# Performance work log

Hardware: AMD Instinct MI355X
Metric: run time of the kernel (lower is better)

Reference implementation:

```python
import jax, jax.numpy as jnp
import numpy as np

DEPTH = 3  # chemprop default message passing depth


def setup_inputs() -> dict:
    key = jax.random.key(0)
    ks = jax.random.split(key, 10)
    n_atoms, n_bonds, max_nb, n_mols = 50000, 100000, 6, 2000
    atom_fdim, bond_fdim, hidden = 133, 147, 300
    f_atoms = jax.random.normal(ks[0], (n_atoms, atom_fdim), dtype=jnp.float32)
    f_bonds = jax.random.normal(ks[1], (n_bonds, bond_fdim), dtype=jnp.float32)
    a2b = jax.random.randint(ks[2], (n_atoms, max_nb), 0, n_bonds, dtype=jnp.int32)
    b2a = jax.random.randint(ks[3], (n_bonds,), 0, n_atoms, dtype=jnp.int32)
    b2revb = jax.random.randint(ks[4], (n_bonds,), 0, n_bonds, dtype=jnp.int32)
    mol_id = jnp.sort(jax.random.randint(ks[5], (n_atoms,), 0, n_mols, dtype=jnp.int32))
    W_i = jax.random.normal(ks[6], (bond_fdim, hidden), dtype=jnp.float32) * 0.05
    W_h = jax.random.normal(ks[7], (hidden, hidden), dtype=jnp.float32) * 0.05
    W_o = jax.random.normal(ks[8], (atom_fdim + hidden, hidden), dtype=jnp.float32) * 0.05
    b_o = jnp.zeros((hidden,), dtype=jnp.float32)
    return {"f_atoms": f_atoms, "f_bonds": f_bonds, "a2b": a2b, "b2a": b2a,
            "b2revb": b2revb, "mol_id": mol_id, "n_mols": n_mols,
            "W_i": W_i, "W_h": W_h, "W_o": W_o, "b_o": b_o}


def reference(f_atoms, f_bonds, a2b, b2a, b2revb, mol_id, n_mols, W_i, W_h, W_o, b_o):
    act = jax.nn.relu
    # W_i: bond features -> hidden; message init
    inp = f_bonds @ W_i                      # [n_bonds, h]
    message = act(inp)
    for _ in range(DEPTH - 1):
        nei = message[a2b]                    # [n_atoms, max_nb, h] gather
        a_message = nei.sum(axis=1)           # [n_atoms, h]
        rev = message[b2revb]                 # [n_bonds, h]
        message = a_message[b2a] - rev        # [n_bonds, h]
        message = act(inp + message @ W_h)
    # final atom readout
    a_message = message[a2b].sum(axis=1)      # [n_atoms, h]
    a_input = jnp.concatenate([f_atoms, a_message], axis=1)  # [n_atoms, fa+h]
    atom_hiddens = act(a_input @ W_o + b_o)   # [n_atoms, h]
    # ragged per-molecule mean (a_scope loop -> segment mean)
    sums = jax.ops.segment_sum(atom_hiddens, mol_id, num_segments=n_mols)
    counts = jax.ops.segment_sum(jnp.ones((atom_hiddens.shape[0],), dtype=atom_hiddens.dtype), mol_id, num_segments=n_mols)
    mol_vecs = jnp.where(counts[:, None] > 0, sums / jnp.maximum(counts, 1.0)[:, None], 0.0)
    return mol_vecs
```

## Files before the change

### kernel.cpp

```cpp
#include <hip/hip_runtime.h>
#include <cstddef>

#define H 300
#define RS 304
#define MAXNB 6
#define ASTR 312

typedef __attribute__((ext_vector_type(8)))  short bf16x8;
typedef __attribute__((ext_vector_type(16))) float f32x16;

__device__ __forceinline__ float bf2f(unsigned short u) {
    return __uint_as_float(((unsigned int)u) << 16);
}
__device__ __forceinline__ unsigned short f2bf(float f) {
    unsigned int u = __float_as_uint(f);
    u += 0x7FFFu + ((u >> 16) & 1u);
    return (unsigned short)(u >> 16);
}
__device__ __forceinline__ unsigned int sub2bf(unsigned int a, unsigned int b) {
    float d0 = bf2f((unsigned short)(a & 0xFFFFu)) - bf2f((unsigned short)(b & 0xFFFFu));
    float d1 = bf2f((unsigned short)(a >> 16))     - bf2f((unsigned short)(b >> 16));
    return (unsigned int)f2bf(d0) | ((unsigned int)f2bf(d1) << 16);
}
__device__ __forceinline__ unsigned int relu2(unsigned int w) {
    unsigned int r = w;
    if (w & 0x80000000u) r &= 0x0000FFFFu;
    if (w & 0x00008000u) r &= 0xFFFF0000u;
    return r;
}
__device__ __forceinline__ uint4 relu4(uint4 v) {
    v.x = relu2(v.x); v.y = relu2(v.y); v.z = relu2(v.z); v.w = relu2(v.w);
    return v;
}
__device__ __forceinline__ uint4 subpack4(uint4 a, uint4 b) {
    uint4 r;
    r.x = sub2bf(a.x, b.x); r.y = sub2bf(a.y, b.y);
    r.z = sub2bf(a.z, b.z); r.w = sub2bf(a.w, b.w);
    return r;
}


template<int S>
__global__ void __launch_bounds__(256)
pack_a_f32_c(const float* __restrict__ src, unsigned short* __restrict__ dst,
             int M, int K)
{
    __shared__ unsigned short sm[64 * 152];
    const int m0 = blockIdx.x * 64;
    const int r = threadIdx.x >> 2;
    const int q = threadIdx.x & 3;
    int mv = m0 + r; if (mv >= M) mv = M - 1;
    const float* rowF = src + (size_t)mv * K;
#pragma unroll
    for (int i = 0; i < (S * 4 + 3) / 4; ++i) {
        int c = q + i * 4;
        if (c * 4 < S * 16) {
            unsigned short h[4];
#pragma unroll
            for (int e = 0; e < 4; ++e) {
                int k = c * 4 + e;
                h[e] = (k < K) ? f2bf(rowF[k]) : (unsigned short)0;
            }
            uint2 o;
            o.x = (unsigned int)h[0] | ((unsigned int)h[1] << 16);
            o.y = (unsigned int)h[2] | ((unsigned int)h[3] << 16);
            *(uint2*)&sm[r * 152 + c * 4] = o;
        }
    }
    __syncthreads();
    for (int j = threadIdx.x; j < 2 * S * 64; j += 256) {
        int lane = j & 63;
        int t = j >> 6;
        int s = t % S;
        int mb2 = t / S;
        uint4 v = *(const uint4*)&sm[(mb2 * 32 + (lane & 31)) * 152 + s * 16 + (lane >> 5) * 8];
        int m_blk = blockIdx.x * 2 + mb2;
        *(uint4*)&dst[((size_t)(m_blk * S + s) * 64 + lane) * 8] = v;
    }
}

__global__ void __launch_bounds__(256)
pack_b(const float* __restrict__ src1, const float* __restrict__ src2,
       unsigned short* __restrict__ dst, int K1, int S1, int K2, int SB)
{
    int g = blockIdx.x * 256 + threadIdx.x;
    if (g >= 10 * SB * 64) return;
    int lane = g & 63;
    int t = g >> 6;
    int s = t % SB;
    int n_blk = t / SB;
    int n = n_blk * 32 + (lane & 31);
    unsigned int w[4];
#pragma unroll
    for (int p = 0; p < 4; ++p) {
        unsigned short h[2];
#pragma unroll
        for (int e = 0; e < 2; ++e) {
            int kf = s * 16 + (lane >> 5) * 8 + p * 2 + e;
            float v = 0.0f;
            if (n < H) {
                if (s < S1) {
                    if (kf < K1) v = src1[(size_t)kf * H + n];
                } else {
                    int k2 = kf - S1 * 16;
                    if (k2 < K2) v = src2[(size_t)k2 * H + n];
                }
            }
            h[e] = f2bf(v);
        }
        w[p] = (unsigned int)h[0] | ((unsigned int)h[1] << 16);
    }
    *(uint4*)&dst[(size_t)g * 8] = make_uint4(w[0], w[1], w[2], w[3]);
}

template<int RELU>
__global__ void __launch_bounds__(256)
aggregate_row(const unsigned short* __restrict__ msg, const int* __restrict__ a2b,
              unsigned short* __restrict__ amsg, int n_atoms)
{
    int gid = blockIdx.x * 256 + threadIdx.x;
    int total = n_atoms * 38;
    if (gid >= total) return;
    int atom = gid / 38;
    int g8 = gid - atom * 38;
    const int* nb = a2b + atom * MAXNB;
    float sum[8] = {};
#pragma unroll
    for (int j = 0; j < MAXNB; ++j) {
        int b = nb[j];
        uint4 v = *(const uint4*)&msg[(size_t)b * RS + g8 * 8];
        if (RELU) v = relu4(v);
        unsigned int ww[4] = {v.x, v.y, v.z, v.w};
#pragma unroll
        for (int p = 0; p < 4; ++p) {
            sum[p * 2]     += bf2f((unsigned short)(ww[p] & 0xFFFFu));
            sum[p * 2 + 1] += bf2f((unsigned short)(ww[p] >> 16));
        }
    }
    unsigned int ow[4];
#pragma unroll
    for (int p = 0; p < 4; ++p)
        ow[p] = (unsigned int)f2bf(sum[p * 2]) | ((unsigned int)f2bf(sum[p * 2 + 1]) << 16);
    *(uint4*)&amsg[(size_t)atom * RS + g8 * 8] = make_uint4(ow[0], ow[1], ow[2], ow[3]);
}

template<int S1, int S2, int SBL, int MODE, int RELUMSG>
__global__ void __launch_bounds__(128)
gemm_fused(const unsigned short* __restrict__ A1,
           const unsigned short* __restrict__ amsg,
           const unsigned short* __restrict__ msg,
           const int* __restrict__ b2a, const int* __restrict__ b2revb,
           const unsigned short* __restrict__ Bp,
           const float* __restrict__ bias,
           const unsigned short* __restrict__ inp_add,
           const float* __restrict__ Adense, int Kd,
           unsigned short* __restrict__ out, int M)
{
    __shared__ __align__(16) unsigned short smem[32 * ASTR];

    const int lane  = threadIdx.x & 63;
    const int w     = threadIdx.x >> 6;
    const int cbase = w * 160;
    const int mrow  = lane & 31;
    const int quad  = lane >> 5;
    const int m0    = blockIdx.x * 32;
    const int m_blk = blockIdx.x;
    const int nblk0 = cbase >> 5;

    {
        const int r = threadIdx.x >> 2;
        const int q = threadIdx.x & 3;
        int mm = m0 + r;
        int mv = (mm < M) ? mm : 0;
        if (MODE == 0) {
            if (mm >= M) mv = M - 1;
            const float* rowF = Adense + (size_t)mv * Kd;
#pragma unroll
            for (int i = 0; i < (S2 * 4 + 3) / 4; ++i) {
                int c = q + i * 4;
                if (c * 4 < S2 * 16) {
                    unsigned short h[4];
#pragma unroll
                    for (int e = 0; e < 4; ++e) {
                        int k = c * 4 + e;
                        h[e] = (k < Kd) ? f2bf(rowF[k]) : (unsigned short)0;
                    }
                    uint2 o;
                    o.x = (unsigned int)h[0] | ((unsigned int)h[1] << 16);
                    o.y = (unsigned int)h[2] | ((unsigned int)h[3] << 16);
                    *(uint2*)&smem[r * ASTR + c * 4] = o;
                }
            }
            __syncthreads();
        } else if (MODE == 1 || MODE == 2) {
            const unsigned short* rowA;
            const unsigned short* rowM = nullptr;
            if (MODE == 1) {
                rowA = amsg + (size_t)b2a[mv] * RS;
                rowM = msg  + (size_t)b2revb[mv] * RS;
            } else {
                rowA = amsg + (size_t)mv * RS;
            }
#pragma unroll
            for (int i = 0; i < 10; ++i) {
                int c = q + i * 4;
                if (c < 38) {
                    uint4 o;
                    if (MODE == 1) {
                        uint4 va = *(const uint4*)(rowA + c * 8);
                        uint4 vm = *(const uint4*)(rowM + c * 8);
                        if (RELUMSG) vm = relu4(vm);
                        o = subpack4(va, vm);
                    } else {
                        o = *(const uint4*)(rowA + c * 8);
                    }
                    *(uint4*)&smem[r * ASTR + c * 8] = o;
                }
            }
            __syncthreads();
        }
    }

    f32x16 acc[5];
#pragma unroll
    for (int t = 0; t < 5; ++t)
#pragma unroll
        for (int i = 0; i < 16; ++i) acc[t][i] = 0.0f;

    const unsigned short* pa1 = (S1 > 0) ? (A1 + ((size_t)m_blk * S1 * 64 + lane) * 8) : nullptr;
    const unsigned short* pb  = Bp + ((size_t)nblk0 * SBL * 64 + lane) * 8;

    constexpr int STOT = S1 + S2;

    auto loadA = [&](int s) -> bf16x8 {
        if (s < S1) return *(const bf16x8*)(pa1 + (size_t)s * 512);
        return *(const bf16x8*)&smem[mrow * ASTR + (s - S1) * 16 + quad * 8];
    };

    bf16x8 b0[5], b1[5];
#pragma unroll
    for (int nt = 0; nt < 5; ++nt) b0[nt] = *(const bf16x8*)(pb + ((size_t)nt * SBL + 0) * 512);
    if (STOT > 1) {
#pragma unroll
        for (int nt = 0; nt < 5; ++nt) b1[nt] = *(const bf16x8*)(pb + ((size_t)nt * SBL + 1) * 512);
    }

#pragma unroll
    for (int s = 0; s < STOT; s += 2) {
        bf16x8 a = loadA(s);
        acc[0] = __builtin_amdgcn_mfma_f32_32x32x16_bf16(a, b0[0], acc[0], 0, 0, 0);
        acc[1] = __builtin_amdgcn_mfma_f32_32x32x16_bf16(a, b0[1], acc[1], 0, 0, 0);
        acc[2] = __builtin_amdgcn_mfma_f32_32x32x16_bf16(a, b0[2], acc[2], 0, 0, 0);
        acc[3] = __builtin_amdgcn_mfma_f32_32x32x16_bf16(a, b0[3], acc[3], 0, 0, 0);
        acc[4] = __builtin_amdgcn_mfma_f32_32x32x16_bf16(a, b0[4], acc[4], 0, 0, 0);
        if (s + 2 < STOT) {
#pragma unroll
            for (int nt = 0; nt < 5; ++nt) b0[nt] = *(const bf16x8*)(pb + ((size_t)nt * SBL + s + 2) * 512);
        }
        if (s + 1 < STOT) {
            bf16x8 a2 = loadA(s + 1);
            acc[0] = __builtin_amdgcn_mfma_f32_32x32x16_bf16(a2, b1[0], acc[0], 0, 0, 0);
            acc[1] = __builtin_amdgcn_mfma_f32_32x32x16_bf16(a2, b1[1], acc[1], 0, 0, 0);
            acc[2] = __builtin_amdgcn_mfma_f32_32x32x16_bf16(a2, b1[2], acc[2], 0, 0, 0);
            acc[3] = __builtin_amdgcn_mfma_f32_32x32x16_bf16(a2, b1[3], acc[3], 0, 0, 0);
            acc[4] = __builtin_amdgcn_mfma_f32_32x32x16_bf16(a2, b1[4], acc[4], 0, 0, 0);
            if (s + 3 < STOT) {
#pragma unroll
                for (int nt = 0; nt < 5; ++nt) b1[nt] = *(const bf16x8*)(pb + ((size_t)nt * SBL + s + 3) * 512);
            }
        }
    }

    __syncthreads();

#pragma unroll
    for (int nt = 0; nt < 5; ++nt) {
        int col = cbase + nt * 32 + mrow;
#pragma unroll
        for (int r = 0; r < 16; ++r) {
            int row = (r & 3) + 8 * (r >> 2) + 4 * quad;
            if (col < 308) smem[row * 308 + col] = f2bf(acc[nt][r]);
        }
    }
    __syncthreads();

    for (int idx = threadIdx.x; idx < 32 * 76; idx += 128) {
        int row = idx / 76, gcol = idx - row * 76;
        int mm = m0 + row;
        if (mm >= M) continue;
        int c0 = gcol * 4;
        uint2 raw = *(const uint2*)&smem[row * 308 + c0];
        uint2 o;
        if (MODE == 0) {
            o = raw;
        } else {
            unsigned short h[4] = {(unsigned short)(raw.x & 0xFFFFu), (unsigned short)(raw.x >> 16),
                                   (unsigned short)(raw.y & 0xFFFFu), (unsigned short)(raw.y >> 16)};
            float v[4];
#pragma unroll
            for (int e = 0; e < 4; ++e) v[e] = bf2f(h[e]);
            if (MODE == 1) {
                uint2 iv = *(const uint2*)&inp_add[(size_t)mm * RS + c0];
                v[0] += bf2f((unsigned short)(iv.x & 0xFFFFu));
                v[1] += bf2f((unsigned short)(iv.x >> 16));
                v[2] += bf2f((unsigned short)(iv.y & 0xFFFFu));
                v[3] += bf2f((unsigned short)(iv.y >> 16));
            } else {
#pragma unroll
                for (int e = 0; e < 4; ++e) v[e] += (c0 + e < H) ? bias[c0 + e] : 0.0f;
            }
#pragma unroll
            for (int e = 0; e < 4; ++e) h[e] = f2bf(fmaxf(v[e], 0.0f));
            o.x = (unsigned int)h[0] | ((unsigned int)h[1] << 16);
            o.y = (unsigned int)h[2] | ((unsigned int)h[3] << 16);
        }
        *(uint2*)&out[(size_t)mm * RS + c0] = o;
    }
}

__global__ void __launch_bounds__(128)
segmean_kernel(const unsigned short* __restrict__ ah,
               const int* __restrict__ mol_id, int n_atoms,
               float* __restrict__ out)
{
    int m = blockIdx.x;
    int lo = 0, hi = n_atoms;
    while (lo < hi) { int mid = (lo + hi) >> 1; if (mol_id[mid] < m) lo = mid + 1; else hi = mid; }
    int start = lo;
    hi = n_atoms;
    while (lo < hi) { int mid = (lo + hi) >> 1; if (mol_id[mid] < m + 1) lo = mid + 1; else hi = mid; }
    int end = lo;

    int c = threadIdx.x;
    float a0 = 0.f, a1 = 0.f, a2 = 0.f;
    for (int a = start; a < end; ++a) {
        const unsigned short* row = ah + (size_t)a * RS;
        a0 += bf2f(row[c]);
        a1 += bf2f(row[c + 128]);
        if (c < H - 256) a2 += bf2f(row[c + 256]);
    }
    float inv = (end > start) ? 1.0f / (float)(end - start) : 0.0f;
    float* orow = out + (size_t)m * H;
    orow[c] = a0 * inv;
    orow[c + 128] = a1 * inv;
    if (c < H - 256) orow[c + 256] = a2 * inv;
}

extern "C" void kernel_launch(void* const* d_in, const int* in_sizes, int n_in,
                              void* d_out, int out_size, void* d_ws, size_t ws_size,
                              hipStream_t stream)
{
    const float* f_atoms = (const float*)d_in[0];
    const float* f_bonds = (const float*)d_in[1];
    const int*   a2b     = (const int*)d_in[2];
    const int*   b2a     = (const int*)d_in[3];
    const int*   b2revb  = (const int*)d_in[4];
    const int*   mol_id  = (const int*)d_in[5];
    const float* W_i     = (const float*)d_in[7];
    const float* W_h     = (const float*)d_in[8];
    const float* W_o     = (const float*)d_in[9];
    const float* b_o     = (const float*)d_in[10];

    const int n_atoms   = in_sizes[5];
    const int n_bonds   = in_sizes[3];
    const int atom_fdim = in_sizes[0] / n_atoms;
    const int bond_fdim = in_sizes[1] / n_bonds;
    const int n_mols    = out_size / H;

    const int gAtoms  = (n_atoms + 63) / 64;
    const int gB32    = (n_bonds + 31) / 32;
    const int gA32    = (n_atoms + 31) / 32;

    const size_t bondsRS = (size_t)n_bonds * RS;
    const size_t atomsRS = (size_t)n_atoms * RS;
    const size_t wihSz   = 10 * 30 * 512;
    const size_t woSz    = 10 * 29 * 512;
    const size_t wh19Sz  = 10 * 19 * 512;

    unsigned short* inp  = (unsigned short*)d_ws;
    unsigned short* msgB = inp  + bondsRS;
    unsigned short* amsg = msgB + bondsRS;
    unsigned short* wih  = amsg + atomsRS;
    unsigned short* wo   = wih  + wihSz;
    unsigned short* wh19 = wo   + woSz;
    unsigned short* ah   = wh19 + wh19Sz;
    unsigned short* fap  = inp;

    dim3 blk(256);
    dim3 gblk(128);
    const int aggBlocks = (n_atoms * 38 + 255) / 256;

    pack_b<<<(10 * 30 * 64 + 255) / 256, blk, 0, stream>>>(W_i, W_h, wih, bond_fdim, 10, H, 30);
    pack_b<<<(10 * 19 * 64 + 255) / 256, blk, 0, stream>>>(W_h, W_h, wh19, H, 19, 0, 19);
    pack_b<<<(10 * 29 * 64 + 255) / 256, blk, 0, stream>>>(W_o, W_o + (size_t)atom_fdim * H, wo,
                                                           atom_fdim, 9, H, 29);

    gemm_fused<0, 10, 30, 0, 0><<<gB32, gblk, 0, stream>>>(
        nullptr, nullptr, nullptr, nullptr, nullptr, wih, nullptr, nullptr,
        f_bonds, bond_fdim, inp, n_bonds);

    aggregate_row<1><<<aggBlocks, blk, 0, stream>>>(inp, a2b, amsg, n_atoms);
    gemm_fused<0, 19, 19, 1, 1><<<gB32, gblk, 0, stream>>>(
        nullptr, amsg, inp, b2a, b2revb, wh19, nullptr, inp, nullptr, 0, msgB, n_bonds);

    aggregate_row<0><<<aggBlocks, blk, 0, stream>>>(msgB, a2b, amsg, n_atoms);
    gemm_fused<0, 19, 19, 1, 0><<<gB32, gblk, 0, stream>>>(
        nullptr, amsg, msgB, b2a, b2revb, wh19, nullptr, inp, nullptr, 0, inp, n_bonds);

    aggregate_row<0><<<aggBlocks, blk, 0, stream>>>(inp, a2b, amsg, n_atoms);

    pack_a_f32_c<9><<<gAtoms, blk, 0, stream>>>(f_atoms, fap, n_atoms, atom_fdim);

    gemm_fused<9, 19, 29, 2, 0><<<gA32, gblk, 0, stream>>>(
        fap, amsg, nullptr, nullptr, nullptr, wo, b_o, nullptr, nullptr, 0, ah, n_atoms);

    segmean_kernel<<<n_mols, dim3(128), 0, stream>>>(ah, mol_id, n_atoms, (float*)d_out);
}
```

Before: 571.8 us.

## Retile fused GEMM to 64-row blocks with ten waves, one N-tile per wave

The fused MFMA GEMM now runs 640-thread blocks over 64 rows instead of 128-thread blocks over 32 rows. Each of the ten waves owns one 32-column output tile and computes two 32-row M tiles that share its B fragment. Before, each of two waves held five B fragments and five accumulators. The aim is to cut per-wave register pressure and give each block more waves to hide latency. In exchange, A is read from LDS twice per B load, 128 threads sit idle during the staging phase, and there are fewer, larger blocks.

```diff
diff --git a/kernel.cpp b/kernel.cpp
--- a/kernel.cpp
+++ b/kernel.cpp
@@ -145,7 +145,7 @@
 }
 
 template<int S1, int S2, int SBL, int MODE, int RELUMSG>
-__global__ void __launch_bounds__(128)
+__global__ void __launch_bounds__(640)
 gemm_fused(const unsigned short* __restrict__ A1,
            const unsigned short* __restrict__ amsg,
            const unsigned short* __restrict__ msg,
@@ -156,28 +156,25 @@
            const float* __restrict__ Adense, int Kd,
            unsigned short* __restrict__ out, int M)
 {
-    __shared__ __align__(16) unsigned short smem[32 * ASTR];
+    __shared__ __align__(16) unsigned short smem[64 * ASTR];
 
     const int lane  = threadIdx.x & 63;
     const int w     = threadIdx.x >> 6;
-    const int cbase = w * 160;
     const int mrow  = lane & 31;
     const int quad  = lane >> 5;
-    const int m0    = blockIdx.x * 32;
-    const int m_blk = blockIdx.x;
-    const int nblk0 = cbase >> 5;
-
-    {
-        const int r = threadIdx.x >> 2;
-        const int q = threadIdx.x & 3;
+    const int m0    = blockIdx.x * 64;
+
+    if (threadIdx.x < 512) {
+        const int r = threadIdx.x >> 3;
+        const int q = threadIdx.x & 7;
         int mm = m0 + r;
         int mv = (mm < M) ? mm : 0;
         if (MODE == 0) {
             if (mm >= M) mv = M - 1;
             const float* rowF = Adense + (size_t)mv * Kd;
 #pragma unroll
-            for (int i = 0; i < (S2 * 4 + 3) / 4; ++i) {
-                int c = q + i * 4;
+            for (int i = 0; i < 5; ++i) {
+                int c = q + i * 8;
                 if (c * 4 < S2 * 16) {
                     unsigned short h[4];
 #pragma unroll
@@ -191,8 +188,7 @@
                     *(uint2*)&smem[r * ASTR + c * 4] = o;
                 }
             }
-            __syncthreads();
-        } else if (MODE == 1 || MODE == 2) {
+        } else {
             const unsigned short* rowA;
             const unsigned short* rowM = nullptr;
             if (MODE == 1) {
@@ -202,8 +198,8 @@
                 rowA = amsg + (size_t)mv * RS;
             }
 #pragma unroll
-            for (int i = 0; i < 10; ++i) {
-                int c = q + i * 4;
+            for (int i = 0; i < 5; ++i) {
+                int c = q + i * 8;
                 if (c < 38) {
                     uint4 o;
                     if (MODE == 1) {
@@ -217,74 +213,67 @@
                     *(uint4*)&smem[r * ASTR + c * 8] = o;
                 }
             }
-            __syncthreads();
-        }
-    }
-
-    f32x16 acc[5];
-#pragma unroll
-    for (int t = 0; t < 5; ++t)
-#pragma unroll
-        for (int i = 0; i < 16; ++i) acc[t][i] = 0.0f;
-
-    const unsigned short* pa1 = (S1 > 0) ? (A1 + ((size_t)m_blk * S1 * 64 + lane) * 8) : nullptr;
-    const unsigned short* pb  = Bp + ((size_t)nblk0 * SBL * 64 + lane) * 8;
+        }
+    }
+    __syncthreads();
+
+    f32x16 acc_lo, acc_hi;
+#pragma unroll
+    for (int i = 0; i < 16; ++i) { acc_lo[i] = 0.0f; acc_hi[i] = 0.0f; }
+
+    const unsigned short* pa1_lo = (S1 > 0)
+        ? (A1 + ((size_t)(blockIdx.x * 2 + 0) * S1 * 64 + lane) * 8) : nullptr;
+    const unsigned short* pa1_hi = (S1 > 0)
+        ? (A1 + ((size_t)(blockIdx.x * 2 + 1) * S1 * 64 + lane) * 8) : nullptr;
+    const unsigned short* pb = Bp + ((size_t)w * SBL * 64 + lane) * 8;
 
     constexpr int STOT = S1 + S2;
 
-    auto loadA = [&](int s) -> bf16x8 {
-        if (s < S1) return *(const bf16x8*)(pa1 + (size_t)s * 512);
-        return *(const bf16x8*)&smem[mrow * ASTR + (s - S1) * 16 + quad * 8];
+    auto loadA = [&](int s, const unsigned short* pa1x, int half) -> bf16x8 {
+        if (s < S1) return *(const bf16x8*)(pa1x + (size_t)s * 512);
+        return *(const bf16x8*)&smem[((half << 5) + mrow) * ASTR + (s - S1) * 16 + quad * 8];
     };
 
-    bf16x8 b0[5], b1[5];
-#pragma unroll
-    for (int nt = 0; nt < 5; ++nt) b0[nt] = *(const bf16x8*)(pb + ((size_t)nt * SBL + 0) * 512);
-    if (STOT > 1) {
-#pragma unroll
-        for (int nt = 0; nt < 5; ++nt) b1[nt] = *(const bf16x8*)(pb + ((size_t)nt * SBL + 1) * 512);
-    }
+    bf16x8 b0, b1;
+    b0 = *(const bf16x8*)(pb);
+    if (STOT > 1) b1 = *(const bf16x8*)(pb + 512);
 
 #pragma unroll
     for (int s = 0; s < STOT; s += 2) {
-        bf16x8 a = loadA(s);
-        acc[0] = __builtin_amdgcn_mfma_f32_32x32x16_bf16(a, b0[0], acc[0], 0, 0, 0);
-        acc[1] = __builtin_amdgcn_mfma_f32_32x32x16_bf16(a, b0[1], acc[1], 0, 0, 0);
-        acc[2] = __builtin_amdgcn_mfma_f32_32x32x16_bf16(a, b0[2], acc[2], 0, 0, 0);
-        acc[3] = __builtin_amdgcn_mfma_f32_32x32x16_bf16(a, b0[3], acc[3], 0, 0, 0);
-        acc[4] = __builtin_amdgcn_mfma_f32_32x32x16_bf16(a, b0[4], acc[4], 0, 0, 0);
-        if (s + 2 < STOT) {
-#pragma unroll
-            for (int nt = 0; nt < 5; ++nt) b0[nt] = *(const bf16x8*)(pb + ((size_t)nt * SBL + s + 2) * 512);
-        }
+        bf16x8 a_lo = loadA(s, pa1_lo, 0);
+        bf16x8 a_hi = loadA(s, pa1_hi, 1);
+        acc_lo = __builtin_amdgcn_mfma_f32_32x32x16_bf16(a_lo, b0, acc_lo, 0, 0, 0);
+        acc_hi = __builtin_amdgcn_mfma_f32_32x32x16_bf16(a_hi, b0, acc_hi, 0, 0, 0);
+        if (s + 2 < STOT) b0 = *(const bf16x8*)(pb + (size_t)(s + 2) * 512);
         if (s + 1 < STOT) {
-            bf16x8 a2 = loadA(s + 1);
-            acc[0] = __builtin_amdgcn_mfma_f32_32x32x16_bf16(a2, b1[0], acc[0], 0, 0, 0);
-            acc[1] = __builtin_amdgcn_mfma_f32_32x32x16_bf16(a2, b1[1], acc[1], 0, 0, 0);
-            acc[2] = __builtin_amdgcn_mfma_f32_32x32x16_bf16(a2, b1[2], acc[2], 0, 0, 0);
-            acc[3] = __builtin_amdgcn_mfma_f32_32x32x16_bf16(a2, b1[3], acc[3], 0, 0, 0);
-            acc[4] = __builtin_amdgcn_mfma_f32_32x32x16_bf16(a2, b1[4], acc[4], 0, 0, 0);
-            if (s + 3 < STOT) {
-#pragma unroll
-                for (int nt = 0; nt < 5; ++nt) b1[nt] = *(const bf16x8*)(pb + ((size_t)nt * SBL + s + 3) * 512);
-            }
+            bf16x8 a_lo2 = loadA(s + 1, pa1_lo, 0);
+            bf16x8 a_hi2 = loadA(s + 1, pa1_hi, 1);
+            acc_lo = __builtin_amdgcn_mfma_f32_32x32x16_bf16(a_lo2, b1, acc_lo, 0, 0, 0);
+            acc_hi = __builtin_amdgcn_mfma_f32_32x32x16_bf16(a_hi2, b1, acc_hi, 0, 0, 0);
+            if (s + 3 < STOT) b1 = *(const bf16x8*)(pb + (size_t)(s + 3) * 512);
         }
     }
 
     __syncthreads();
 
-#pragma unroll
-    for (int nt = 0; nt < 5; ++nt) {
-        int col = cbase + nt * 32 + mrow;
-#pragma unroll
-        for (int r = 0; r < 16; ++r) {
-            int row = (r & 3) + 8 * (r >> 2) + 4 * quad;
-            if (col < 308) smem[row * 308 + col] = f2bf(acc[nt][r]);
+    {
+        int col = w * 32 + mrow;
+        if (col < 308) {
+#pragma unroll
+            for (int r = 0; r < 16; ++r) {
+                int row = (r & 3) + 8 * (r >> 2) + 4 * quad;
+                smem[row * 308 + col] = f2bf(acc_lo[r]);
+            }
+#pragma unroll
+            for (int r = 0; r < 16; ++r) {
+                int row = 32 + (r & 3) + 8 * (r >> 2) + 4 * quad;
+                smem[row * 308 + col] = f2bf(acc_hi[r]);
+            }
         }
     }
     __syncthreads();
 
-    for (int idx = threadIdx.x; idx < 32 * 76; idx += 128) {
+    for (int idx = threadIdx.x; idx < 64 * 76; idx += 640) {
         int row = idx / 76, gcol = idx - row * 76;
         int mm = m0 + row;
         if (mm >= M) continue;
@@ -368,8 +357,7 @@
     const int n_mols    = out_size / H;
 
     const int gAtoms  = (n_atoms + 63) / 64;
-    const int gB32    = (n_bonds + 31) / 32;
-    const int gA32    = (n_atoms + 31) / 32;
+    const int gBonds  = (n_bonds + 63) / 64;
 
     const size_t bondsRS = (size_t)n_bonds * RS;
     const size_t atomsRS = (size_t)n_atoms * RS;
@@ -387,7 +375,7 @@
     unsigned short* fap  = inp;
 
     dim3 blk(256);
-    dim3 gblk(128);
+    dim3 gblk(640);
     const int aggBlocks = (n_atoms * 38 + 255) / 256;
 
     pack_b<<<(10 * 30 * 64 + 255) / 256, blk, 0, stream>>>(W_i, W_h, wih, bond_fdim, 10, H, 30);
@@ -395,23 +383,23 @@
     pack_b<<<(10 * 29 * 64 + 255) / 256, blk, 0, stream>>>(W_o, W_o + (size_t)atom_fdim * H, wo,
                                                            atom_fdim, 9, H, 29);
 
-    gemm_fused<0, 10, 30, 0, 0><<<gB32, gblk, 0, stream>>>(
+    gemm_fused<0, 10, 30, 0, 0><<<gBonds, gblk, 0, stream>>>(
         nullptr, nullptr, nullptr, nullptr, nullptr, wih, nullptr, nullptr,
         f_bonds, bond_fdim, inp, n_bonds);
 
     aggregate_row<1><<<aggBlocks, blk, 0, stream>>>(inp, a2b, amsg, n_atoms);
-    gemm_fused<0, 19, 19, 1, 1><<<gB32, gblk, 0, stream>>>(
+    gemm_fused<0, 19, 19, 1, 1><<<gBonds, gblk, 0, stream>>>(
         nullptr, amsg, inp, b2a, b2revb, wh19, nullptr, inp, nullptr, 0, msgB, n_bonds);
 
     aggregate_row<0><<<aggBlocks, blk, 0, stream>>>(msgB, a2b, amsg, n_atoms);
-    gemm_fused<0, 19, 19, 1, 0><<<gB32, gblk, 0, stream>>>(
+    gemm_fused<0, 19, 19, 1, 0><<<gBonds, gblk, 0, stream>>>(
         nullptr, amsg, msgB, b2a, b2revb, wh19, nullptr, inp, nullptr, 0, inp, n_bonds);
 
     aggregate_row<0><<<aggBlocks, blk, 0, stream>>>(inp, a2b, amsg, n_atoms);
 
     pack_a_f32_c<9><<<gAtoms, blk, 0, stream>>>(f_atoms, fap, n_atoms, atom_fdim);
 
-    gemm_fused<9, 19, 29, 2, 0><<<gA32, gblk, 0, stream>>>(
+    gemm_fused<9, 19, 29, 2, 0><<<gAtoms, gblk, 0, stream>>>(
         fap, amsg, nullptr, nullptr, nullptr, wo, b_o, nullptr, nullptr, 0, ah, n_atoms);
 
     segmean_kernel<<<n_mols, dim3(128), 0, stream>>>(ah, mol_id, n_atoms, (float*)d_out);
```

Result: faster. 487.5 us (-14.7%).
